# Kernel tuning notes

Measured on AMD Instinct MI355X. Metric: run time of the kernel, lower is better.

Reference implementation:

```python
import math
import jax, jax.numpy as jnp
import numpy as np

EMBED, HEADS, LEVELS, POINTS = 256, 8, 4, 4
HEAD_DIM = EMBED // HEADS
SHAPES = ((100, 100), (50, 50), (25, 25), (13, 13))  # (h, w) per level
BS, NQ = 8, 900
NV = sum(h * w for h, w in SHAPES)


def _offset_bias():
    # Faithful to init_weights(): per-head rotated grid init for sampling_offsets bias.
    th = np.arange(HEADS, dtype=np.float32) * (2.0 * math.pi / HEADS)
    g = np.stack([np.cos(th), np.sin(th)], -1)
    g = g / np.abs(g).max(-1, keepdims=True)
    g = np.tile(g[:, None, None, :], (1, LEVELS, POINTS, 1))
    g = g * (np.arange(POINTS, dtype=np.float32) + 1.0)[None, None, :, None]
    return jnp.asarray(g.reshape(-1))


def setup_inputs() -> dict:
    key = jax.random.key(0)
    ks = jax.random.split(key, 10)
    s = 0.05
    return {
        "query": jax.random.normal(ks[0], (BS, NQ, EMBED), jnp.float32),
        "value": jax.random.normal(ks[1], (BS, NV, EMBED), jnp.float32),
        "reference_points": jax.random.uniform(ks[2], (BS, NQ, LEVELS, 2), jnp.float32),
        "spatial_shapes": jnp.array(SHAPES, jnp.int32),
        "W_off": jax.random.normal(ks[3], (EMBED, HEADS * LEVELS * POINTS * 2), jnp.float32) * s,
        "b_off": _offset_bias(),
        "W_attn": jax.random.normal(ks[4], (EMBED, HEADS * LEVELS * POINTS), jnp.float32) * s,
        "b_attn": jnp.zeros((HEADS * LEVELS * POINTS,), jnp.float32),
        "W_v": jax.random.normal(ks[5], (EMBED, EMBED), jnp.float32) * s,
        "b_v": jnp.zeros((EMBED,), jnp.float32),
        "W_out": jax.random.normal(ks[6], (EMBED, EMBED), jnp.float32) * s,
        "b_out": jnp.zeros((EMBED,), jnp.float32),
    }


def _bilinear_sample(vl, loc, H, W, aw):
    """grid_sample bilinear, align_corners=False, zero padding, fused with attn weights.

    vl:  (bs, heads, H*W, d)   loc: (bs, nq, heads, P, 2) in [0,1] (x, y)
    aw:  (bs, heads, nq, P)    ->   (bs, heads, nq, d)
    """
    x = loc[..., 0] * W - 0.5
    y = loc[..., 1] * H - 0.5
    x0 = jnp.floor(x)
    y0 = jnp.floor(y)
    lx = x - x0
    ly = y - y0
    x0i = x0.astype(jnp.int32)
    y0i = y0.astype(jnp.int32)
    bs, heads = vl.shape[0], vl.shape[1]
    nq, P = loc.shape[1], loc.shape[3]
    acc = jnp.zeros((bs, heads, nq, vl.shape[-1]), vl.dtype)
    corners = ((0, 0, (1 - lx) * (1 - ly)), (1, 0, lx * (1 - ly)),
               (0, 1, (1 - lx) * ly), (1, 1, lx * ly))
    for dx, dy, wgt in corners:
        xi = x0i + dx
        yi = y0i + dy
        valid = ((xi >= 0) & (xi < W) & (yi >= 0) & (yi < H)).astype(vl.dtype)
        idx = jnp.clip(yi, 0, H - 1) * W + jnp.clip(xi, 0, W - 1)  # (bs, nq, heads, P)
        idx = idx.transpose(0, 2, 1, 3).reshape(bs, heads, nq * P)
        g = jnp.take_along_axis(vl, idx[..., None], axis=2).reshape(bs, heads, nq, P, -1)
        cw = (wgt * valid).transpose(0, 2, 1, 3) * aw  # (bs, heads, nq, P)
        acc = acc + (g * cw[..., None]).sum(3)
    return acc


def reference(query, value, reference_points, spatial_shapes,
              W_off, b_off, W_attn, b_attn, W_v, b_v, W_out, b_out):
    identity = query
    bs, nq, _ = query.shape
    v = (value @ W_v + b_v).reshape(bs, -1, HEADS, HEAD_DIM)
    off = (query @ W_off + b_off).reshape(bs, nq, HEADS, LEVELS, POINTS, 2)
    aw = (query @ W_attn + b_attn).reshape(bs, nq, HEADS, LEVELS * POINTS)
    aw = jax.nn.softmax(aw, -1).reshape(bs, nq, HEADS, LEVELS, POINTS)
    # offset normalizer is (w, h) per level
    norm = jnp.stack([spatial_shapes[:, 1], spatial_shapes[:, 0]], -1).astype(query.dtype)
    loc = reference_points[:, :, None, :, None, :] + off / norm[None, None, None, :, None, :]
    sizes = [h * w for h, w in SHAPES]
    starts = np.cumsum([0] + sizes[:-1])
    out = jnp.zeros((bs, HEADS, nq, HEAD_DIM), query.dtype)
    for l, (h, w) in enumerate(SHAPES):
        vl = jax.lax.dynamic_slice_in_dim(v, int(starts[l]), sizes[l], axis=1)
        vl = vl.transpose(0, 2, 1, 3)  # (bs, heads, h*w, d)
        aw_l = aw[:, :, :, l].transpose(0, 2, 1, 3)  # (bs, heads, nq, P)
        out = out + _bilinear_sample(vl, loc[:, :, :, l], h, w, aw_l)
    out = out.transpose(0, 2, 1, 3).reshape(bs, nq, EMBED)
    return out @ W_out + b_out + identity
```

## Files before the change

### kernel.cpp

```cpp
#include <hip/hip_runtime.h>
#include <hip/hip_bf16.h>

#define EMBED    256
#define HEADS    8
#define LEVELS   4
#define POINTS   4
#define HEAD_DIM 32
#define BS       8
#define NQ       900
#define NV       13294
#define MV       (BS*NV)
#define MQ       (BS*NQ)
#define NQOUT    384

typedef float  f32x4  __attribute__((ext_vector_type(4)));
typedef __bf16 bf16x8 __attribute__((ext_vector_type(8)));
typedef unsigned short ushort8  __attribute__((ext_vector_type(8)));
typedef unsigned short ushort4v __attribute__((ext_vector_type(4)));

__device__ __forceinline__ unsigned short f2bf(float f) {
    unsigned u = __builtin_bit_cast(unsigned, f);
    u += 0x7FFFu + ((u >> 16) & 1u);
    return (unsigned short)(u >> 16);
}
__device__ __forceinline__ float bf2f(unsigned short h) {
    unsigned u = ((unsigned)h) << 16;
    return __builtin_bit_cast(float, u);
}

__global__ __launch_bounds__(256) void prep_kernel(
    const float* __restrict__ Wv,  const float* __restrict__ Woff,
    const float* __restrict__ Wattn, const float* __restrict__ Wout,
    const float* __restrict__ boff, const float* __restrict__ battn,
    unsigned short* __restrict__ WtV, unsigned short* __restrict__ WtQ,
    unsigned short* __restrict__ WtO, float* __restrict__ biasQ)
{
    int n = blockIdx.x;
    int k = threadIdx.x;
    if (n < 256) {
        WtV[n * 256 + k] = f2bf(Wv [k * 256 + n]);
        WtO[n * 256 + k] = f2bf(Wout[k * 256 + n]);
        WtQ[n * 256 + k] = f2bf(Woff[k * 256 + n]);
    } else {
        int j = n - 256;
        WtQ[n * 256 + k] = f2bf(Wattn[k * 128 + j]);
    }
    if (k == 0) biasQ[n] = (n < 256) ? boff[n] : battn[n - 256];
}

template <int WPB, bool OUT_BF16, bool ADD_ID>
__global__ __launch_bounds__(WPB * 64, 1)
void gemm_regw(const float* __restrict__ A,
               const unsigned short* __restrict__ Bt,
               const float* __restrict__ bias,
               const float* __restrict__ Ident,
               void* __restrict__ Cv, int M)
{
    constexpr int N = WPB * 64;
    const int tid  = threadIdx.x;
    const int wave = tid >> 6, lane = tid & 63;
    const int lrow = lane & 15, kq = lane >> 4;
    const int n0   = wave * 64;

    bf16x8 wf[4][8];
    #pragma unroll
    for (int j = 0; j < 4; ++j)
        #pragma unroll
        for (int c = 0; c < 8; ++c)
            wf[j][c] = *(const bf16x8*)(Bt + (size_t)(n0 + j * 16 + lrow) * 256
                                           + c * 32 + kq * 8);
    f32x4 bj[4];
    #pragma unroll
    for (int j = 0; j < 4; ++j)
        bj[j] = *(const f32x4*)(bias + n0 + j * 16 + kq * 4);

    const int NS    = M / 16;
    const int chunk = (NS + gridDim.x - 1) / gridDim.x;
    const int sbeg  = blockIdx.x * chunk;
    const int send  = min(NS, sbeg + chunk);

    for (int s = sbeg; s < send; ++s) {
        const float* abase = A + (size_t)(s * 16 + lrow) * 256 + kq * 8;
        f32x4 pa[16];
        #pragma unroll
        for (int c = 0; c < 8; ++c) {
            pa[2 * c]     = *(const f32x4*)(abase + c * 32);
            pa[2 * c + 1] = *(const f32x4*)(abase + c * 32 + 4);
        }
        f32x4 acc[4];
        #pragma unroll
        for (int j = 0; j < 4; ++j) acc[j] = (f32x4)0.f;

        #pragma unroll
        for (int c = 0; c < 8; ++c) {
            ushort8 vb;
            #pragma unroll
            for (int e = 0; e < 4; ++e) {
                vb[e]     = f2bf(pa[2 * c][e]);
                vb[4 + e] = f2bf(pa[2 * c + 1][e]);
            }
            bf16x8 vf = __builtin_bit_cast(bf16x8, vb);
            #pragma unroll
            for (int j = 0; j < 4; ++j)
                acc[j] = __builtin_amdgcn_mfma_f32_16x16x32_bf16(
                    wf[j][c], vf, acc[j], 0, 0, 0);
        }

        const size_t crow = (size_t)(s * 16 + lrow) * N + n0 + kq * 4;
        #pragma unroll
        for (int j = 0; j < 4; ++j) {
            f32x4 r = acc[j] + bj[j];
            if (ADD_ID)
                r += *(const f32x4*)(Ident + crow + j * 16);
            if (OUT_BF16) {
                ushort4v o;
                #pragma unroll
                for (int e = 0; e < 4; ++e) o[e] = f2bf(r[e]);
                *(ushort4v*)((unsigned short*)Cv + crow + j * 16) = o;
            } else {
                *(f32x4*)((float*)Cv + crow + j * 16) = r;
            }
        }
    }
}

__device__ const int   LVL_W[4]  = {100, 50, 25, 13};
__device__ const int   LVL_H[4]  = {100, 50, 25, 13};
__device__ const int   LVL_S[4]  = {0, 10000, 12500, 13125};

__global__ __launch_bounds__(256) void sample_kernel(
    const unsigned short* __restrict__ V,
    const float* __restrict__ Qout,
    const float* __restrict__ RP,
    float* __restrict__ OutS)
{
    const int gid = blockIdx.x * 16 + (threadIdx.x >> 4);
    const int s   = threadIdx.x & 15;
    const int h   = gid & 7;
    const int bq  = gid >> 3;
    const int b   = bq / NQ;

    const float* qrow = Qout + (size_t)bq * NQOUT;

    const int l = s >> 2;
    const float ox = qrow[h * 32 + 2 * s];
    const float oy = qrow[h * 32 + 2 * s + 1];
    float logit    = qrow[256 + h * 16 + s];
    const float rpx = RP[((size_t)bq * 4 + l) * 2 + 0];
    const float rpy = RP[((size_t)bq * 4 + l) * 2 + 1];
    int W = LVL_W[l], H = LVL_H[l], st = LVL_S[l];
    float x = rpx * (float)W + ox - 0.5f;
    float y = rpy * (float)H + oy - 0.5f;
    float fx = floorf(x), fy = floorf(y);
    float lx = x - fx, ly = y - fy;
    int ix = (int)fx, iy = (int)fy;

    float mx = logit;
    #pragma unroll
    for (int o = 8; o; o >>= 1) mx = fmaxf(mx, __shfl_xor(mx, o, 16));
    float e = __expf(logit - mx);
    float sum = e;
    #pragma unroll
    for (int o = 8; o; o >>= 1) sum += __shfl_xor(sum, o, 16);
    const float wgt = e / sum;

    const unsigned short* vb = V + ((size_t)b * NV) * 256 + h * 32 + 2 * s;
    float ax = 0.f, ay = 0.f;

    #pragma unroll
    for (int sp = 0; sp < 16; ++sp) {
        float ws  = __shfl(wgt, sp, 16);
        float lxs = __shfl(lx,  sp, 16);
        float lys = __shfl(ly,  sp, 16);
        int  ixs  = __shfl(ix,  sp, 16);
        int  iys  = __shfl(iy,  sp, 16);
        int  Ws   = __shfl(W,   sp, 16);
        int  Hs   = __shfl(H,   sp, 16);
        int  sts  = __shfl(st,  sp, 16);
        #pragma unroll
        for (int corner = 0; corner < 4; ++corner) {
            int dx = corner & 1, dy = corner >> 1;
            int xi = ixs + dx, yi = iys + dy;
            float cw = ws * (dx ? lxs : 1.f - lxs) * (dy ? lys : 1.f - lys);
            if (xi >= 0 && xi < Ws && yi >= 0 && yi < Hs && cw != 0.f) {
                const unsigned short* p = vb + (size_t)(sts + yi * Ws + xi) * 256;
                unsigned pv = *(const unsigned*)p;
                ax += cw * bf2f((unsigned short)(pv & 0xFFFF));
                ay += cw * bf2f((unsigned short)(pv >> 16));
            }
        }
    }
    float2* o = (float2*)(OutS + (size_t)bq * 256 + h * 32);
    o[s] = make_float2(ax, ay);
}

extern "C" void kernel_launch(void* const* d_in, const int* in_sizes, int n_in,
                              void* d_out, int out_size, void* d_ws, size_t ws_size,
                              hipStream_t stream)
{
    const float* query  = (const float*)d_in[0];
    const float* value  = (const float*)d_in[1];
    const float* rp     = (const float*)d_in[2];
    const float* W_off  = (const float*)d_in[4];
    const float* b_off  = (const float*)d_in[5];
    const float* W_attn = (const float*)d_in[6];
    const float* b_attn = (const float*)d_in[7];
    const float* W_v    = (const float*)d_in[8];
    const float* b_v    = (const float*)d_in[9];
    const float* W_out  = (const float*)d_in[10];
    const float* b_out  = (const float*)d_in[11];

    char* ws = (char*)d_ws;
    size_t off = 0;
    unsigned short* Vbf = (unsigned short*)(ws + off); off += (size_t)MV * 256 * 2;
    float* qout         = (float*)(ws + off);          off += (size_t)MQ * NQOUT * 4;
    float* outs         = (float*)(ws + off);          off += (size_t)MQ * 256 * 4;
    unsigned short* WtV = (unsigned short*)(ws + off); off += 256 * 256 * 2;
    unsigned short* WtQ = (unsigned short*)(ws + off); off += 384 * 256 * 2;
    unsigned short* WtO = (unsigned short*)(ws + off); off += 256 * 256 * 2;
    float* biasQ        = (float*)(ws + off);          off += 384 * 4;

    prep_kernel<<<384, 256, 0, stream>>>(W_v, W_off, W_attn, W_out, b_off, b_attn,
                                         WtV, WtQ, WtO, biasQ);

    gemm_regw<4, true, false><<<512, 256, 0, stream>>>(
        value, WtV, b_v, nullptr, Vbf, MV);

    gemm_regw<6, false, false><<<225, 384, 0, stream>>>(
        query, WtQ, biasQ, nullptr, qout, MQ);

    sample_kernel<<<(BS * NQ * HEADS) / 16, 256, 0, stream>>>(Vbf, qout, rp, outs);

    gemm_regw<4, false, true><<<225, 256, 0, stream>>>(
        outs, WtO, b_out, query, (float*)d_out, MQ);
}
```

Before: 308.8 us.

## Double-buffer GEMM A strips, branchless bilinear gather, and double GEMM grid sizes

The register-weight GEMM now prefetches the next 16-row A strip into a second register buffer while the current strip is converted and fed to MFMA, so global load latency overlaps compute. The sampling kernel replaces its bounds-checked conditional loads with clamped, always-issued loads scaled by a validity mask, and splits the accumulation across two FMA chains. The query and output GEMM grids grow from 225 to 450 blocks for more parallelism. The costs are higher register pressure from the second buffer, extra loads for out-of-range and zero-weight corners, and fewer strips per block, which shortens the prefetch pipeline.

```diff
diff --git a/kernel.cpp b/kernel.cpp
--- a/kernel.cpp
+++ b/kernel.cpp
@@ -49,48 +49,28 @@
 }
 
 template <int WPB, bool OUT_BF16, bool ADD_ID>
-__global__ __launch_bounds__(WPB * 64, 1)
-void gemm_regw(const float* __restrict__ A,
-               const unsigned short* __restrict__ Bt,
-               const float* __restrict__ bias,
-               const float* __restrict__ Ident,
-               void* __restrict__ Cv, int M)
-{
-    constexpr int N = WPB * 64;
-    const int tid  = threadIdx.x;
-    const int wave = tid >> 6, lane = tid & 63;
-    const int lrow = lane & 15, kq = lane >> 4;
-    const int n0   = wave * 64;
-
-    bf16x8 wf[4][8];
-    #pragma unroll
-    for (int j = 0; j < 4; ++j)
-        #pragma unroll
-        for (int c = 0; c < 8; ++c)
-            wf[j][c] = *(const bf16x8*)(Bt + (size_t)(n0 + j * 16 + lrow) * 256
-                                           + c * 32 + kq * 8);
-    f32x4 bj[4];
-    #pragma unroll
-    for (int j = 0; j < 4; ++j)
-        bj[j] = *(const f32x4*)(bias + n0 + j * 16 + kq * 4);
-
-    const int NS    = M / 16;
-    const int chunk = (NS + gridDim.x - 1) / gridDim.x;
-    const int sbeg  = blockIdx.x * chunk;
-    const int send  = min(NS, sbeg + chunk);
-
-    for (int s = sbeg; s < send; ++s) {
-        const float* abase = A + (size_t)(s * 16 + lrow) * 256 + kq * 8;
-        f32x4 pa[16];
+struct GemmOps {
+    static constexpr int N = WPB * 64;
+
+    __device__ static void load_strip(f32x4 (&pa)[16], const float* __restrict__ A,
+                                      int s, int lrow, int kq) {
+        const float* ab = A + (size_t)(s * 16 + lrow) * 256 + kq * 8;
         #pragma unroll
         for (int c = 0; c < 8; ++c) {
-            pa[2 * c]     = *(const f32x4*)(abase + c * 32);
-            pa[2 * c + 1] = *(const f32x4*)(abase + c * 32 + 4);
-        }
+            pa[2 * c]     = *(const f32x4*)(ab + c * 32);
+            pa[2 * c + 1] = *(const f32x4*)(ab + c * 32 + 4);
+        }
+    }
+
+    __device__ static void compute_store(const f32x4 (&pa)[16],
+                                         const bf16x8 (&wf)[4][8],
+                                         const f32x4 (&bj)[4],
+                                         const float* __restrict__ Ident,
+                                         void* __restrict__ Cv,
+                                         int s, int lrow, int kq, int n0) {
         f32x4 acc[4];
         #pragma unroll
         for (int j = 0; j < 4; ++j) acc[j] = (f32x4)0.f;
-
         #pragma unroll
         for (int c = 0; c < 8; ++c) {
             ushort8 vb;
@@ -105,7 +85,6 @@
                 acc[j] = __builtin_amdgcn_mfma_f32_16x16x32_bf16(
                     wf[j][c], vf, acc[j], 0, 0, 0);
         }
-
         const size_t crow = (size_t)(s * 16 + lrow) * N + n0 + kq * 4;
         #pragma unroll
         for (int j = 0; j < 4; ++j) {
@@ -122,6 +101,50 @@
             }
         }
     }
+};
+
+template <int WPB, bool OUT_BF16, bool ADD_ID>
+__global__ __launch_bounds__(WPB * 64, 1)
+void gemm_regw(const float* __restrict__ A,
+               const unsigned short* __restrict__ Bt,
+               const float* __restrict__ bias,
+               const float* __restrict__ Ident,
+               void* __restrict__ Cv, int M)
+{
+    using Ops = GemmOps<WPB, OUT_BF16, ADD_ID>;
+    const int tid  = threadIdx.x;
+    const int wave = tid >> 6, lane = tid & 63;
+    const int lrow = lane & 15, kq = lane >> 4;
+    const int n0   = wave * 64;
+
+    bf16x8 wf[4][8];
+    #pragma unroll
+    for (int j = 0; j < 4; ++j)
+        #pragma unroll
+        for (int c = 0; c < 8; ++c)
+            wf[j][c] = *(const bf16x8*)(Bt + (size_t)(n0 + j * 16 + lrow) * 256
+                                           + c * 32 + kq * 8);
+    f32x4 bj[4];
+    #pragma unroll
+    for (int j = 0; j < 4; ++j)
+        bj[j] = *(const f32x4*)(bias + n0 + j * 16 + kq * 4);
+
+    const int NS    = M / 16;
+    const int chunk = (NS + gridDim.x - 1) / gridDim.x;
+    const int sbeg  = blockIdx.x * chunk;
+    const int send  = min(NS, sbeg + chunk);
+    if (sbeg >= send) return;
+
+    f32x4 buf0[16], buf1[16];
+    Ops::load_strip(buf0, A, sbeg, lrow, kq);
+    for (int s = sbeg; s < send; s += 2) {
+        if (s + 1 < send) Ops::load_strip(buf1, A, s + 1, lrow, kq);
+        Ops::compute_store(buf0, wf, bj, Ident, Cv, s, lrow, kq, n0);
+        if (s + 1 < send) {
+            if (s + 2 < send) Ops::load_strip(buf0, A, s + 2, lrow, kq);
+            Ops::compute_store(buf1, wf, bj, Ident, Cv, s + 1, lrow, kq, n0);
+        }
+    }
 }
 
 __device__ const int   LVL_W[4]  = {100, 50, 25, 13};
@@ -165,7 +188,7 @@
     const float wgt = e / sum;
 
     const unsigned short* vb = V + ((size_t)b * NV) * 256 + h * 32 + 2 * s;
-    float ax = 0.f, ay = 0.f;
+    float ax0 = 0.f, ay0 = 0.f, ax1 = 0.f, ay1 = 0.f;
 
     #pragma unroll
     for (int sp = 0; sp < 16; ++sp) {
@@ -181,17 +204,23 @@
         for (int corner = 0; corner < 4; ++corner) {
             int dx = corner & 1, dy = corner >> 1;
             int xi = ixs + dx, yi = iys + dy;
-            float cw = ws * (dx ? lxs : 1.f - lxs) * (dy ? lys : 1.f - lys);
-            if (xi >= 0 && xi < Ws && yi >= 0 && yi < Hs && cw != 0.f) {
-                const unsigned short* p = vb + (size_t)(sts + yi * Ws + xi) * 256;
-                unsigned pv = *(const unsigned*)p;
-                ax += cw * bf2f((unsigned short)(pv & 0xFFFF));
-                ay += cw * bf2f((unsigned short)(pv >> 16));
+            float valid = (xi >= 0 && xi < Ws && yi >= 0 && yi < Hs) ? 1.f : 0.f;
+            int xc = min(max(xi, 0), Ws - 1);
+            int yc = min(max(yi, 0), Hs - 1);
+            float cw = ws * (dx ? lxs : 1.f - lxs) * (dy ? lys : 1.f - lys) * valid;
+            const unsigned short* p = vb + (size_t)(sts + yc * Ws + xc) * 256;
+            unsigned pv = *(const unsigned*)p;
+            if (corner & 1) {
+                ax1 = fmaf(cw, bf2f((unsigned short)(pv & 0xFFFF)), ax1);
+                ay1 = fmaf(cw, bf2f((unsigned short)(pv >> 16)), ay1);
+            } else {
+                ax0 = fmaf(cw, bf2f((unsigned short)(pv & 0xFFFF)), ax0);
+                ay0 = fmaf(cw, bf2f((unsigned short)(pv >> 16)), ay0);
             }
         }
     }
     float2* o = (float2*)(OutS + (size_t)bq * 256 + h * 32);
-    o[s] = make_float2(ax, ay);
+    o[s] = make_float2(ax0 + ax1, ay0 + ay1);
 }
 
 extern "C" void kernel_launch(void* const* d_in, const int* in_sizes, int n_in,
@@ -226,11 +255,11 @@
     gemm_regw<4, true, false><<<512, 256, 0, stream>>>(
         value, WtV, b_v, nullptr, Vbf, MV);
 
-    gemm_regw<6, false, false><<<225, 384, 0, stream>>>(
+    gemm_regw<6, false, false><<<450, 384, 0, stream>>>(
         query, WtQ, biasQ, nullptr, qout, MQ);
 
     sample_kernel<<<(BS * NQ * HEADS) / 16, 256, 0, stream>>>(Vbf, qout, rp, outs);
 
-    gemm_regw<4, false, true><<<225, 256, 0, stream>>>(
+    gemm_regw<4, false, true><<<450, 256, 0, stream>>>(
         outs, WtO, b_out, query, (float*)d_out, MQ);
 }
```

New measurement: 317.6 us. +2.8%, slower.
